# Kernel optimization log

Measured on AMD Instinct MI355X. Metric: run time of the kernel, lower is better.

The kernel has to match this reference:

```python
import jax, jax.numpy as jnp
import numpy as np

N_QUBITS = 4
N_LAYERS = 2
_I2 = jnp.eye(2, dtype=jnp.complex64)
_X = jnp.array([[0.0, 1.0], [1.0, 0.0]], dtype=jnp.complex64)


def _apply_1q_batched(state, U, wire):
    # state: [B,2,2,2,2] complex, U: [B,2,2] (per-sample gate)
    s = jnp.moveaxis(state, 1 + wire, -1)
    s = jnp.einsum('bij,b...j->b...i', U, s)
    return jnp.moveaxis(s, -1, 1 + wire)


def _apply_1q(state, U, wire):
    # shared 2x2 gate on `wire`
    s = jnp.moveaxis(state, 1 + wire, -1)
    s = jnp.einsum('ij,...j->...i', U, s)
    return jnp.moveaxis(s, -1, 1 + wire)


def _apply_cnot(state, c, t):
    s = jnp.moveaxis(state, (1 + c, 1 + t), (-2, -1))  # [...,2(ctrl),2(tgt)]
    s = jnp.stack([s[..., 0, :], s[..., 1, ::-1]], axis=-2)  # flip target if ctrl=1
    return jnp.moveaxis(s, (-2, -1), (1 + c, 1 + t))


def _rot_matrix(phi, theta, omega):
    # qml.Rot = RZ(omega) @ RY(theta) @ RZ(phi)
    c, s = jnp.cos(theta / 2), jnp.sin(theta / 2)
    ep = jnp.exp(-0.5j * (phi + omega))  # e^{-i(phi+omega)/2}
    em = jnp.exp(-0.5j * (phi - omega))  # e^{-i(phi-omega)/2}
    return jnp.stack([
        jnp.stack([ep * c, -jnp.conj(em) * s]),
        jnp.stack([em * s, jnp.conj(ep) * c]),
    ]).astype(jnp.complex64)


def _circuit(angles, weights):
    # angles: [B, 4] real; weights: [2, 4, 3] real -> [B, 4] PauliZ expvals
    B = angles.shape[0]
    state = jnp.zeros((B,) + (2,) * N_QUBITS, jnp.complex64)
    state = state.at[(slice(None),) + (0,) * N_QUBITS].set(1.0)  # |0000>
    # AngleEmbedding (rotation='X'): RX(angle_w) on wire w, batched over samples
    for w in range(N_QUBITS):
        half = angles[:, w] / 2
        c, s = jnp.cos(half), jnp.sin(half)
        U = c[:, None, None] * _I2 - 1j * s[:, None, None] * _X  # [B,2,2]
        state = _apply_1q_batched(state, U, w)
    # StronglyEntanglingLayers: Rot on each wire, then ring of CNOTs with range r
    for l in range(N_LAYERS):
        for w in range(N_QUBITS):
            U = _rot_matrix(weights[l, w, 0], weights[l, w, 1], weights[l, w, 2])
            state = _apply_1q(state, U, w)
        r = (l % (N_QUBITS - 1)) + 1  # PennyLane default ranges
        for w in range(N_QUBITS):
            state = _apply_cnot(state, w, (w + r) % N_QUBITS)
    probs = state.real ** 2 + state.imag ** 2  # [B,2,2,2,2]
    z = []
    for w in range(N_QUBITS):
        other = tuple(a for a in range(1, N_QUBITS + 1) if a != 1 + w)
        p = probs.sum(other)  # [B,2]
        z.append(p[:, 0] - p[:, 1])
    return jnp.stack(z, axis=-1)  # [B,4]


def setup_inputs() -> dict:
    key = jax.random.key(0)
    ks = jax.random.split(key, 6)
    B, D_IN, D_OUT, NQ = 65536, 512, 512, N_QUBITS
    x = jax.random.normal(ks[0], (B, D_IN), jnp.float32)
    pre_W = jax.random.normal(ks[1], (NQ, D_IN), jnp.float32) / np.sqrt(D_IN)
    pre_b = jax.random.normal(ks[2], (NQ,), jnp.float32) * 0.05
    weights = jax.random.uniform(ks[3], (N_LAYERS, NQ, 3), jnp.float32) * (2 * np.pi)
    post_W = jax.random.normal(ks[4], (D_OUT, NQ), jnp.float32) / np.sqrt(NQ)
    post_b = jax.random.normal(ks[5], (D_OUT,), jnp.float32) * 0.05
    return {"x": x, "pre_W": pre_W, "pre_b": pre_b, "weights": weights,
            "post_W": post_W, "post_b": post_b}


def reference(x, pre_W, pre_b, weights, post_W, post_b):
    angles = jnp.tanh(x @ pre_W.T + pre_b) * jnp.pi  # [B,4]
    q = _circuit(angles, weights)                    # [B,4]
    return q @ post_W.T + post_b                     # [B,512]
```

## Files before the change

### kernel.cpp

```cpp
#include <hip/hip_runtime.h>
#include <math.h>

#define PI_F 3.14159265358979323846f


typedef float floatx4 __attribute__((ext_vector_type(4)));

static __device__ __forceinline__ void st_store4(float* p, floatx4 v)
{
    *reinterpret_cast<floatx4*>(p) = v;
}

static __device__ __forceinline__ float fast_tanh(float a)
{
    a = fminf(fmaxf(a, -15.f), 15.f);
    const float e = __expf(2.f * a);
    return (e - 1.f) / (e + 1.f);
}

template<int ST>
__device__ __forceinline__ void rot_inlane(float* ar, float* ai,
    float u00r, float u00i, float u01r, float u01i,
    float u10r, float u10i, float u11r, float u11i)
{
#pragma unroll
    for (int k = 0; k < 4; ++k) {
        if (k & ST) continue;
        const int j = k | ST;
        const float Ar = ar[k], Ai = ai[k], Br = ar[j], Bi = ai[j];
        ar[k] = u00r*Ar - u00i*Ai + u01r*Br - u01i*Bi;
        ai[k] = u00r*Ai + u00i*Ar + u01r*Bi + u01i*Br;
        ar[j] = u10r*Ar - u10i*Ai + u11r*Br - u11i*Bi;
        ai[j] = u10r*Ai + u10i*Ar + u11r*Bi + u11i*Br;
    }
}

template<int XM>
__device__ __forceinline__ void rot_cross(float* ar, float* ai, bool ownB,
    float u00r, float u00i, float u01r, float u01i,
    float u10r, float u10i, float u11r, float u11i)
{
    const float cAr = ownB ? u11r : u00r;
    const float cAi = ownB ? u11i : u00i;
    const float cBr = ownB ? u10r : u01r;
    const float cBi = ownB ? u10i : u01i;
#pragma unroll
    for (int k = 0; k < 4; ++k) {
        const float pr = __shfl_xor(ar[k], XM, 64);
        const float pi = __shfl_xor(ai[k], XM, 64);
        const float vr = ar[k], vi = ai[k];
        ar[k] = cAr*vr - cAi*vi + cBr*pr - cBi*pi;
        ai[k] = cAr*vi + cAi*vr + cBr*pi + cBi*pr;
    }
}

#define ROT_COEFFS(L, W) \
    const float ph = wts[((L)*4+(W))*3+0]; \
    const float th = wts[((L)*4+(W))*3+1]; \
    const float om = wts[((L)*4+(W))*3+2]; \
    const float s_  = __sinf(0.5f*th),        c_  = __cosf(0.5f*th); \
    const float sp_ = __sinf(0.5f*(ph+om)),   cp_ = __cosf(0.5f*(ph+om)); \
    const float sq_ = __sinf(0.5f*(ph-om)),   cq_ = __cosf(0.5f*(ph-om));

#define U_ARGS cp_*c_, -sp_*c_, -cq_*s_, -sq_*s_, cq_*s_, -sq_*s_, cp_*c_, sp_*c_

__global__ __launch_bounds__(256) void k_fused(
    const float* __restrict__ x,
    const float* __restrict__ preW,
    const float* __restrict__ preb,
    const float* __restrict__ wts,
    const float* __restrict__ postW,
    const float* __restrict__ postb,
    float* __restrict__ out, int B)
{
    const int lane  = threadIdx.x & 63;
    const int wid   = threadIdx.x >> 6;
    const int base  = blockIdx.x * 64;
    const int wbase = base + wid * 16;
    if (base >= B) return;

    float4 wA[4], wB[4];
#pragma unroll
    for (int w = 0; w < 4; ++w) {
        wA[w] = *reinterpret_cast<const float4*>(preW + w * 512 + lane * 4);
        wB[w] = *reinterpret_cast<const float4*>(preW + w * 512 + 256 + lane * 4);
    }
    const float4 pb = *reinterpret_cast<const float4*>(preb);
    const float pb01 = (lane & 1) ? pb.y : pb.x;
    const float pb23 = (lane & 1) ? pb.w : pb.z;
    const float pbv  = (lane & 2) ? pb23 : pb01;

    float a[4];
#pragma unroll
    for (int p = 0; p < 4; ++p) {
        const int b0 = wbase + p * 4;

        float4 xa[4], xb[4];
#pragma unroll
        for (int t = 0; t < 4; ++t) {
            const float* xr = x + (size_t)(b0 + t) * 512;
            xa[t] = *reinterpret_cast<const float4*>(xr + lane * 4);
            xb[t] = *reinterpret_cast<const float4*>(xr + 256 + lane * 4);
        }

        float acc[4][4];
#pragma unroll
        for (int t = 0; t < 4; ++t) {
#pragma unroll
            for (int w = 0; w < 4; ++w) {
                acc[t][w] = xa[t].x * wA[w].x + xa[t].y * wA[w].y + xa[t].z * wA[w].z + xa[t].w * wA[w].w
                          + xb[t].x * wB[w].x + xb[t].y * wB[w].y + xb[t].z * wB[w].z + xb[t].w * wB[w].w;
            }
        }

        float v[4];
#pragma unroll
        for (int t = 0; t < 4; ++t) {
            float a01 = (lane & 1) ? acc[t][1] : acc[t][0];
            float b01 = (lane & 1) ? acc[t][0] : acc[t][1];
            a01 += __shfl_xor(b01, 1, 64);
            float a23 = (lane & 1) ? acc[t][3] : acc[t][2];
            float b23 = (lane & 1) ? acc[t][2] : acc[t][3];
            a23 += __shfl_xor(b23, 1, 64);
            const float vv = (lane & 2) ? a23 : a01;
            const float uu = (lane & 2) ? a01 : a23;
            v[t] = vv + __shfl_xor(uu, 2, 64);
        }
        float c01 = (lane & 4) ? v[1] : v[0];
        float d01 = (lane & 4) ? v[0] : v[1];
        c01 += __shfl_xor(d01, 4, 64);
        float c23 = (lane & 4) ? v[3] : v[2];
        float d23 = (lane & 4) ? v[2] : v[3];
        c23 += __shfl_xor(d23, 4, 64);
        float m = (lane & 8) ? c23 : c01;
        float n = (lane & 8) ? c01 : c23;
        m += __shfl_xor(n, 8, 64);
        m += __shfl_xor(m, 16, 64);
        m += __shfl_xor(m, 32, 64);

        a[p] = fast_tanh(m + pbv) * PI_F;
    }

    const float comb = (lane & 32) ? ((lane & 16) ? a[3] : a[2])
                                   : ((lane & 16) ? a[1] : a[0]);
    const int sb = (lane & 48) + 4 * ((lane >> 2) & 3);
    const float A0 = __shfl(comb, sb + 0, 64);
    const float A1 = __shfl(comb, sb + 1, 64);
    const float A2 = __shfl(comb, sb + 2, 64);
    const float A3 = __shfl(comb, sb + 3, 64);

    const bool lb3 = (lane & 2) != 0;
    const bool lb2 = (lane & 1) != 0;

    const float s0 = __sinf(0.5f * A0), c0 = __cosf(0.5f * A0);
    const float s1 = __sinf(0.5f * A1), c1 = __cosf(0.5f * A1);
    const float s2 = __sinf(0.5f * A2), c2 = __cosf(0.5f * A2);
    const float s3 = __sinf(0.5f * A3), c3 = __cosf(0.5f * A3);

    const float mhi = (lb3 ? s0 : c0) * (lb2 ? s1 : c1);
    const float hr  = lb3 ? (lb2 ? -mhi : 0.f) : (lb2 ? 0.f : mhi);
    const float hi  = (lb3 != lb2) ? -mhi : 0.f;
    const float low0 = c2 * c3, low1 = c2 * s3, low2 = s2 * c3, low3 = s2 * s3;

    float ar[4], ai[4];
    ar[0] =  hr * low0;  ai[0] =  hi * low0;
    ar[1] =  hi * low1;  ai[1] = -hr * low1;
    ar[2] =  hi * low2;  ai[2] = -hr * low2;
    ar[3] = -hr * low3;  ai[3] = -hi * low3;

    { ROT_COEFFS(0, 0); rot_cross<2>(ar, ai, lb3, U_ARGS); }
    { ROT_COEFFS(0, 1); rot_cross<1>(ar, ai, lb2, U_ARGS); }
    { ROT_COEFFS(0, 2); rot_inlane<2>(ar, ai, U_ARGS); }
    { ROT_COEFFS(0, 3); rot_inlane<1>(ar, ai, U_ARGS); }

    {
#pragma unroll
        for (int k = 0; k < 4; ++k) {
            const float tr = __shfl_xor(ar[k], 1, 64);
            const float ti = __shfl_xor(ai[k], 1, 64);
            ar[k] = lb3 ? tr : ar[k];
            ai[k] = lb3 ? ti : ai[k];
        }
    }
    {
        const float t0r = ar[0], t0i = ai[0], t1r = ar[1], t1i = ai[1];
        ar[0] = lb2 ? ar[2] : ar[0];  ai[0] = lb2 ? ai[2] : ai[0];
        ar[1] = lb2 ? ar[3] : ar[1];  ai[1] = lb2 ? ai[3] : ai[1];
        ar[2] = lb2 ? t0r   : ar[2];  ai[2] = lb2 ? t0i   : ai[2];
        ar[3] = lb2 ? t1r   : ar[3];  ai[3] = lb2 ? t1i   : ai[3];
    }
    {
        float t;
        t = ar[2]; ar[2] = ar[3]; ar[3] = t;
        t = ai[2]; ai[2] = ai[3]; ai[3] = t;
    }
    {
        ar[1] = __shfl_xor(ar[1], 2, 64);  ai[1] = __shfl_xor(ai[1], 2, 64);
        ar[3] = __shfl_xor(ar[3], 2, 64);  ai[3] = __shfl_xor(ai[3], 2, 64);
    }

    { ROT_COEFFS(1, 0); rot_cross<2>(ar, ai, lb3, U_ARGS); }
    { ROT_COEFFS(1, 1); rot_cross<1>(ar, ai, lb2, U_ARGS); }
    { ROT_COEFFS(1, 2); rot_inlane<2>(ar, ai, U_ARGS); }
    { ROT_COEFFS(1, 3); rot_inlane<1>(ar, ai, U_ARGS); }

    {
        const float t0r = ar[0], t0i = ai[0], t1r = ar[1], t1i = ai[1];
        ar[0] = lb3 ? ar[2] : ar[0];  ai[0] = lb3 ? ai[2] : ai[0];
        ar[1] = lb3 ? ar[3] : ar[1];  ai[1] = lb3 ? ai[3] : ai[1];
        ar[2] = lb3 ? t0r   : ar[2];  ai[2] = lb3 ? t0i   : ai[2];
        ar[3] = lb3 ? t1r   : ar[3];  ai[3] = lb3 ? t1i   : ai[3];
    }
    {
        const float t0r = ar[0], t0i = ai[0], t2r = ar[2], t2i = ai[2];
        ar[0] = lb2 ? ar[1] : ar[0];  ai[0] = lb2 ? ai[1] : ai[0];
        ar[1] = lb2 ? t0r   : ar[1];  ai[1] = lb2 ? t0i   : ai[1];
        ar[2] = lb2 ? ar[3] : ar[2];  ai[2] = lb2 ? ai[3] : ai[2];
        ar[3] = lb2 ? t2r   : ar[3];  ai[3] = lb2 ? t2i   : ai[3];
    }
    {
        ar[2] = __shfl_xor(ar[2], 2, 64);  ai[2] = __shfl_xor(ai[2], 2, 64);
        ar[3] = __shfl_xor(ar[3], 2, 64);  ai[3] = __shfl_xor(ai[3], 2, 64);
    }
    {
        ar[1] = __shfl_xor(ar[1], 1, 64);  ai[1] = __shfl_xor(ai[1], 1, 64);
        ar[3] = __shfl_xor(ar[3], 1, 64);  ai[3] = __shfl_xor(ai[3], 1, 64);
    }

    const float p0 = ar[0]*ar[0] + ai[0]*ai[0];
    const float p1 = ar[1]*ar[1] + ai[1]*ai[1];
    const float p2 = ar[2]*ar[2] + ai[2]*ai[2];
    const float p3 = ar[3]*ar[3] + ai[3]*ai[3];
    const float s01 = p0 + p1, s23 = p2 + p3;
    const float sum = s01 + s23;
    float z0 = lb3 ? -sum : sum;
    float z1 = lb2 ? -sum : sum;
    float z2 = s01 - s23;
    float z3 = (p0 - p1) + (p2 - p3);
    z0 += __shfl_xor(z0, 1, 64);  z0 += __shfl_xor(z0, 2, 64);
    z1 += __shfl_xor(z1, 1, 64);  z1 += __shfl_xor(z1, 2, 64);
    z2 += __shfl_xor(z2, 1, 64);  z2 += __shfl_xor(z2, 2, 64);
    z3 += __shfl_xor(z3, 1, 64);  z3 += __shfl_xor(z3, 2, 64);

    const float4* pW4 = reinterpret_cast<const float4*>(postW);
    const float4* pb4 = reinterpret_cast<const float4*>(postb);
    const float4 q0w = pW4[4 * lane + 0], q1w = pW4[4 * lane + 1];
    const float4 q2w = pW4[4 * lane + 2], q3w = pW4[4 * lane + 3];
    const float4 q4w = pW4[4 * (64 + lane) + 0], q5w = pW4[4 * (64 + lane) + 1];
    const float4 q6w = pW4[4 * (64 + lane) + 2], q7w = pW4[4 * (64 + lane) + 3];
    const float4 bb0 = pb4[lane], bb1 = pb4[64 + lane];

#pragma unroll
    for (int s = 0; s < 16; ++s) {
        const float q0 = __shfl(z0, s * 4, 64);
        const float q1 = __shfl(z1, s * 4, 64);
        const float q2 = __shfl(z2, s * 4, 64);
        const float q3 = __shfl(z3, s * 4, 64);
        floatx4 o0, o1;
        o0.x = fmaf(q3, q0w.w, fmaf(q2, q0w.z, fmaf(q1, q0w.y, fmaf(q0, q0w.x, bb0.x))));
        o0.y = fmaf(q3, q1w.w, fmaf(q2, q1w.z, fmaf(q1, q1w.y, fmaf(q0, q1w.x, bb0.y))));
        o0.z = fmaf(q3, q2w.w, fmaf(q2, q2w.z, fmaf(q1, q2w.y, fmaf(q0, q2w.x, bb0.z))));
        o0.w = fmaf(q3, q3w.w, fmaf(q2, q3w.z, fmaf(q1, q3w.y, fmaf(q0, q3w.x, bb0.w))));
        o1.x = fmaf(q3, q4w.w, fmaf(q2, q4w.z, fmaf(q1, q4w.y, fmaf(q0, q4w.x, bb1.x))));
        o1.y = fmaf(q3, q5w.w, fmaf(q2, q5w.z, fmaf(q1, q5w.y, fmaf(q0, q5w.x, bb1.y))));
        o1.z = fmaf(q3, q6w.w, fmaf(q2, q6w.z, fmaf(q1, q6w.y, fmaf(q0, q6w.x, bb1.z))));
        o1.w = fmaf(q3, q7w.w, fmaf(q2, q7w.z, fmaf(q1, q7w.y, fmaf(q0, q7w.x, bb1.w))));
        float* orow = out + (size_t)(wbase + s) * 512;
        st_store4(orow + 4 * lane, o0);
        st_store4(orow + 256 + 4 * lane, o1);
    }
}

extern "C" void kernel_launch(void* const* d_in, const int* in_sizes, int n_in,
                              void* d_out, int out_size, void* d_ws, size_t ws_size,
                              hipStream_t stream)
{
    const float* x     = (const float*)d_in[0];
    const float* preW  = (const float*)d_in[1];
    const float* preb  = (const float*)d_in[2];
    const float* wts   = (const float*)d_in[3];
    const float* postW = (const float*)d_in[4];
    const float* postb = (const float*)d_in[5];
    float* out = (float*)d_out;
    const int B = in_sizes[0] / 512;

    k_fused<<<dim3((B + 63) / 64), dim3(256), 0, stream>>>(
        x, preW, preb, wts, postW, postb, out, B);
}
```

Measured before the change: 48.10 us.

## Double-buffer x row loads and process two 16-row chunks per wave

Each wave now handles 32 rows instead of 16, split into two 16-row chunks. The x loads for the next 4-row pass are issued into a second register buffer while the current pass's dot products and reductions run, so global-load latency overlaps with compute. The per-wave weight loads are amortized over twice as many rows and the grid is halved. The cost is higher register pressure from the double buffer, which may reduce occupancy.

```diff
diff --git a/kernel.cpp b/kernel.cpp
--- a/kernel.cpp
+++ b/kernel.cpp
@@ -5,11 +5,6 @@
 
 
 typedef float floatx4 __attribute__((ext_vector_type(4)));
-
-static __device__ __forceinline__ void st_store4(float* p, floatx4 v)
-{
-    *reinterpret_cast<floatx4*>(p) = v;
-}
 
 static __device__ __forceinline__ float fast_tanh(float a)
 {
@@ -64,6 +59,55 @@
 
 #define U_ARGS cp_*c_, -sp_*c_, -cq_*s_, -sq_*s_, cq_*s_, -sq_*s_, cp_*c_, sp_*c_
 
+#define ISSUE_PASS(slot, p) { \
+    const float* xr_ = x + (size_t)(wbase + (p) * 4) * 512 + lane * 4; \
+    bxa[slot][0] = *reinterpret_cast<const float4*>(xr_); \
+    bxb[slot][0] = *reinterpret_cast<const float4*>(xr_ + 256); \
+    bxa[slot][1] = *reinterpret_cast<const float4*>(xr_ + 512); \
+    bxb[slot][1] = *reinterpret_cast<const float4*>(xr_ + 768); \
+    bxa[slot][2] = *reinterpret_cast<const float4*>(xr_ + 1024); \
+    bxb[slot][2] = *reinterpret_cast<const float4*>(xr_ + 1280); \
+    bxa[slot][3] = *reinterpret_cast<const float4*>(xr_ + 1536); \
+    bxb[slot][3] = *reinterpret_cast<const float4*>(xr_ + 1792); }
+
+#define DOTS_FOLD(slot, dest) { \
+    float acc[4][4]; \
+    _Pragma("unroll") \
+    for (int t = 0; t < 4; ++t) { \
+        _Pragma("unroll") \
+        for (int w = 0; w < 4; ++w) { \
+            acc[t][w] = bxa[slot][t].x * wA[w].x + bxa[slot][t].y * wA[w].y \
+                      + bxa[slot][t].z * wA[w].z + bxa[slot][t].w * wA[w].w \
+                      + bxb[slot][t].x * wB[w].x + bxb[slot][t].y * wB[w].y \
+                      + bxb[slot][t].z * wB[w].z + bxb[slot][t].w * wB[w].w; \
+        } \
+    } \
+    float v[4]; \
+    _Pragma("unroll") \
+    for (int t = 0; t < 4; ++t) { \
+        float a01 = (lane & 1) ? acc[t][1] : acc[t][0]; \
+        float b01 = (lane & 1) ? acc[t][0] : acc[t][1]; \
+        a01 += __shfl_xor(b01, 1, 64); \
+        float a23 = (lane & 1) ? acc[t][3] : acc[t][2]; \
+        float b23 = (lane & 1) ? acc[t][2] : acc[t][3]; \
+        a23 += __shfl_xor(b23, 1, 64); \
+        const float vv = (lane & 2) ? a23 : a01; \
+        const float uu = (lane & 2) ? a01 : a23; \
+        v[t] = vv + __shfl_xor(uu, 2, 64); \
+    } \
+    float c01 = (lane & 4) ? v[1] : v[0]; \
+    float d01 = (lane & 4) ? v[0] : v[1]; \
+    c01 += __shfl_xor(d01, 4, 64); \
+    float c23 = (lane & 4) ? v[3] : v[2]; \
+    float d23 = (lane & 4) ? v[2] : v[3]; \
+    c23 += __shfl_xor(d23, 4, 64); \
+    float m_ = (lane & 8) ? c23 : c01; \
+    float n_ = (lane & 8) ? c01 : c23; \
+    m_ += __shfl_xor(n_, 8, 64); \
+    m_ += __shfl_xor(m_, 16, 64); \
+    m_ += __shfl_xor(m_, 32, 64); \
+    dest = fast_tanh(m_ + pbv) * PI_F; }
+
 __global__ __launch_bounds__(256) void k_fused(
     const float* __restrict__ x,
     const float* __restrict__ preW,
@@ -75,9 +119,8 @@
 {
     const int lane  = threadIdx.x & 63;
     const int wid   = threadIdx.x >> 6;
-    const int base  = blockIdx.x * 64;
-    const int wbase = base + wid * 16;
-    if (base >= B) return;
+    const int wbase = blockIdx.x * 128 + wid * 32;
+    if (wbase >= B) return;
 
     float4 wA[4], wB[4];
 #pragma unroll
@@ -90,158 +133,6 @@
     const float pb23 = (lane & 1) ? pb.w : pb.z;
     const float pbv  = (lane & 2) ? pb23 : pb01;
 
-    float a[4];
-#pragma unroll
-    for (int p = 0; p < 4; ++p) {
-        const int b0 = wbase + p * 4;
-
-        float4 xa[4], xb[4];
-#pragma unroll
-        for (int t = 0; t < 4; ++t) {
-            const float* xr = x + (size_t)(b0 + t) * 512;
-            xa[t] = *reinterpret_cast<const float4*>(xr + lane * 4);
-            xb[t] = *reinterpret_cast<const float4*>(xr + 256 + lane * 4);
-        }
-
-        float acc[4][4];
-#pragma unroll
-        for (int t = 0; t < 4; ++t) {
-#pragma unroll
-            for (int w = 0; w < 4; ++w) {
-                acc[t][w] = xa[t].x * wA[w].x + xa[t].y * wA[w].y + xa[t].z * wA[w].z + xa[t].w * wA[w].w
-                          + xb[t].x * wB[w].x + xb[t].y * wB[w].y + xb[t].z * wB[w].z + xb[t].w * wB[w].w;
-            }
-        }
-
-        float v[4];
-#pragma unroll
-        for (int t = 0; t < 4; ++t) {
-            float a01 = (lane & 1) ? acc[t][1] : acc[t][0];
-            float b01 = (lane & 1) ? acc[t][0] : acc[t][1];
-            a01 += __shfl_xor(b01, 1, 64);
-            float a23 = (lane & 1) ? acc[t][3] : acc[t][2];
-            float b23 = (lane & 1) ? acc[t][2] : acc[t][3];
-            a23 += __shfl_xor(b23, 1, 64);
-            const float vv = (lane & 2) ? a23 : a01;
-            const float uu = (lane & 2) ? a01 : a23;
-            v[t] = vv + __shfl_xor(uu, 2, 64);
-        }
-        float c01 = (lane & 4) ? v[1] : v[0];
-        float d01 = (lane & 4) ? v[0] : v[1];
-        c01 += __shfl_xor(d01, 4, 64);
-        float c23 = (lane & 4) ? v[3] : v[2];
-        float d23 = (lane & 4) ? v[2] : v[3];
-        c23 += __shfl_xor(d23, 4, 64);
-        float m = (lane & 8) ? c23 : c01;
-        float n = (lane & 8) ? c01 : c23;
-        m += __shfl_xor(n, 8, 64);
-        m += __shfl_xor(m, 16, 64);
-        m += __shfl_xor(m, 32, 64);
-
-        a[p] = fast_tanh(m + pbv) * PI_F;
-    }
-
-    const float comb = (lane & 32) ? ((lane & 16) ? a[3] : a[2])
-                                   : ((lane & 16) ? a[1] : a[0]);
-    const int sb = (lane & 48) + 4 * ((lane >> 2) & 3);
-    const float A0 = __shfl(comb, sb + 0, 64);
-    const float A1 = __shfl(comb, sb + 1, 64);
-    const float A2 = __shfl(comb, sb + 2, 64);
-    const float A3 = __shfl(comb, sb + 3, 64);
-
-    const bool lb3 = (lane & 2) != 0;
-    const bool lb2 = (lane & 1) != 0;
-
-    const float s0 = __sinf(0.5f * A0), c0 = __cosf(0.5f * A0);
-    const float s1 = __sinf(0.5f * A1), c1 = __cosf(0.5f * A1);
-    const float s2 = __sinf(0.5f * A2), c2 = __cosf(0.5f * A2);
-    const float s3 = __sinf(0.5f * A3), c3 = __cosf(0.5f * A3);
-
-    const float mhi = (lb3 ? s0 : c0) * (lb2 ? s1 : c1);
-    const float hr  = lb3 ? (lb2 ? -mhi : 0.f) : (lb2 ? 0.f : mhi);
-    const float hi  = (lb3 != lb2) ? -mhi : 0.f;
-    const float low0 = c2 * c3, low1 = c2 * s3, low2 = s2 * c3, low3 = s2 * s3;
-
-    float ar[4], ai[4];
-    ar[0] =  hr * low0;  ai[0] =  hi * low0;
-    ar[1] =  hi * low1;  ai[1] = -hr * low1;
-    ar[2] =  hi * low2;  ai[2] = -hr * low2;
-    ar[3] = -hr * low3;  ai[3] = -hi * low3;
-
-    { ROT_COEFFS(0, 0); rot_cross<2>(ar, ai, lb3, U_ARGS); }
-    { ROT_COEFFS(0, 1); rot_cross<1>(ar, ai, lb2, U_ARGS); }
-    { ROT_COEFFS(0, 2); rot_inlane<2>(ar, ai, U_ARGS); }
-    { ROT_COEFFS(0, 3); rot_inlane<1>(ar, ai, U_ARGS); }
-
-    {
-#pragma unroll
-        for (int k = 0; k < 4; ++k) {
-            const float tr = __shfl_xor(ar[k], 1, 64);
-            const float ti = __shfl_xor(ai[k], 1, 64);
-            ar[k] = lb3 ? tr : ar[k];
-            ai[k] = lb3 ? ti : ai[k];
-        }
-    }
-    {
-        const float t0r = ar[0], t0i = ai[0], t1r = ar[1], t1i = ai[1];
-        ar[0] = lb2 ? ar[2] : ar[0];  ai[0] = lb2 ? ai[2] : ai[0];
-        ar[1] = lb2 ? ar[3] : ar[1];  ai[1] = lb2 ? ai[3] : ai[1];
-        ar[2] = lb2 ? t0r   : ar[2];  ai[2] = lb2 ? t0i   : ai[2];
-        ar[3] = lb2 ? t1r   : ar[3];  ai[3] = lb2 ? t1i   : ai[3];
-    }
-    {
-        float t;
-        t = ar[2]; ar[2] = ar[3]; ar[3] = t;
-        t = ai[2]; ai[2] = ai[3]; ai[3] = t;
-    }
-    {
-        ar[1] = __shfl_xor(ar[1], 2, 64);  ai[1] = __shfl_xor(ai[1], 2, 64);
-        ar[3] = __shfl_xor(ar[3], 2, 64);  ai[3] = __shfl_xor(ai[3], 2, 64);
-    }
-
-    { ROT_COEFFS(1, 0); rot_cross<2>(ar, ai, lb3, U_ARGS); }
-    { ROT_COEFFS(1, 1); rot_cross<1>(ar, ai, lb2, U_ARGS); }
-    { ROT_COEFFS(1, 2); rot_inlane<2>(ar, ai, U_ARGS); }
-    { ROT_COEFFS(1, 3); rot_inlane<1>(ar, ai, U_ARGS); }
-
-    {
-        const float t0r = ar[0], t0i = ai[0], t1r = ar[1], t1i = ai[1];
-        ar[0] = lb3 ? ar[2] : ar[0];  ai[0] = lb3 ? ai[2] : ai[0];
-        ar[1] = lb3 ? ar[3] : ar[1];  ai[1] = lb3 ? ai[3] : ai[1];
-        ar[2] = lb3 ? t0r   : ar[2];  ai[2] = lb3 ? t0i   : ai[2];
-        ar[3] = lb3 ? t1r   : ar[3];  ai[3] = lb3 ? t1i   : ai[3];
-    }
-    {
-        const float t0r = ar[0], t0i = ai[0], t2r = ar[2], t2i = ai[2];
-        ar[0] = lb2 ? ar[1] : ar[0];  ai[0] = lb2 ? ai[1] : ai[0];
-        ar[1] = lb2 ? t0r   : ar[1];  ai[1] = lb2 ? t0i   : ai[1];
-        ar[2] = lb2 ? ar[3] : ar[2];  ai[2] = lb2 ? ai[3] : ai[2];
-        ar[3] = lb2 ? t2r   : ar[3];  ai[3] = lb2 ? t2i   : ai[3];
-    }
-    {
-        ar[2] = __shfl_xor(ar[2], 2, 64);  ai[2] = __shfl_xor(ai[2], 2, 64);
-        ar[3] = __shfl_xor(ar[3], 2, 64);  ai[3] = __shfl_xor(ai[3], 2, 64);
-    }
-    {
-        ar[1] = __shfl_xor(ar[1], 1, 64);  ai[1] = __shfl_xor(ai[1], 1, 64);
-        ar[3] = __shfl_xor(ar[3], 1, 64);  ai[3] = __shfl_xor(ai[3], 1, 64);
-    }
-
-    const float p0 = ar[0]*ar[0] + ai[0]*ai[0];
-    const float p1 = ar[1]*ar[1] + ai[1]*ai[1];
-    const float p2 = ar[2]*ar[2] + ai[2]*ai[2];
-    const float p3 = ar[3]*ar[3] + ai[3]*ai[3];
-    const float s01 = p0 + p1, s23 = p2 + p3;
-    const float sum = s01 + s23;
-    float z0 = lb3 ? -sum : sum;
-    float z1 = lb2 ? -sum : sum;
-    float z2 = s01 - s23;
-    float z3 = (p0 - p1) + (p2 - p3);
-    z0 += __shfl_xor(z0, 1, 64);  z0 += __shfl_xor(z0, 2, 64);
-    z1 += __shfl_xor(z1, 1, 64);  z1 += __shfl_xor(z1, 2, 64);
-    z2 += __shfl_xor(z2, 1, 64);  z2 += __shfl_xor(z2, 2, 64);
-    z3 += __shfl_xor(z3, 1, 64);  z3 += __shfl_xor(z3, 2, 64);
-
     const float4* pW4 = reinterpret_cast<const float4*>(postW);
     const float4* pb4 = reinterpret_cast<const float4*>(postb);
     const float4 q0w = pW4[4 * lane + 0], q1w = pW4[4 * lane + 1];
@@ -250,25 +141,143 @@
     const float4 q6w = pW4[4 * (64 + lane) + 2], q7w = pW4[4 * (64 + lane) + 3];
     const float4 bb0 = pb4[lane], bb1 = pb4[64 + lane];
 
-#pragma unroll
-    for (int s = 0; s < 16; ++s) {
-        const float q0 = __shfl(z0, s * 4, 64);
-        const float q1 = __shfl(z1, s * 4, 64);
-        const float q2 = __shfl(z2, s * 4, 64);
-        const float q3 = __shfl(z3, s * 4, 64);
-        floatx4 o0, o1;
-        o0.x = fmaf(q3, q0w.w, fmaf(q2, q0w.z, fmaf(q1, q0w.y, fmaf(q0, q0w.x, bb0.x))));
-        o0.y = fmaf(q3, q1w.w, fmaf(q2, q1w.z, fmaf(q1, q1w.y, fmaf(q0, q1w.x, bb0.y))));
-        o0.z = fmaf(q3, q2w.w, fmaf(q2, q2w.z, fmaf(q1, q2w.y, fmaf(q0, q2w.x, bb0.z))));
-        o0.w = fmaf(q3, q3w.w, fmaf(q2, q3w.z, fmaf(q1, q3w.y, fmaf(q0, q3w.x, bb0.w))));
-        o1.x = fmaf(q3, q4w.w, fmaf(q2, q4w.z, fmaf(q1, q4w.y, fmaf(q0, q4w.x, bb1.x))));
-        o1.y = fmaf(q3, q5w.w, fmaf(q2, q5w.z, fmaf(q1, q5w.y, fmaf(q0, q5w.x, bb1.y))));
-        o1.z = fmaf(q3, q6w.w, fmaf(q2, q6w.z, fmaf(q1, q6w.y, fmaf(q0, q6w.x, bb1.z))));
-        o1.w = fmaf(q3, q7w.w, fmaf(q2, q7w.z, fmaf(q1, q7w.y, fmaf(q0, q7w.x, bb1.w))));
-        float* orow = out + (size_t)(wbase + s) * 512;
-        st_store4(orow + 4 * lane, o0);
-        st_store4(orow + 256 + 4 * lane, o1);
-    }
+    const bool lb3 = (lane & 2) != 0;
+    const bool lb2 = (lane & 1) != 0;
+    const int  sb  = (lane & 48) + 4 * ((lane >> 2) & 3);
+
+    float4 bxa[2][4], bxb[2][4];
+
+    auto chunk_body = [&](int cb, float a0, float a1, float a2, float a3) {
+        const float comb = (lane & 32) ? ((lane & 16) ? a3 : a2)
+                                       : ((lane & 16) ? a1 : a0);
+        const float A0 = __shfl(comb, sb + 0, 64);
+        const float A1 = __shfl(comb, sb + 1, 64);
+        const float A2 = __shfl(comb, sb + 2, 64);
+        const float A3 = __shfl(comb, sb + 3, 64);
+
+        const float s0 = __sinf(0.5f * A0), c0 = __cosf(0.5f * A0);
+        const float s1 = __sinf(0.5f * A1), c1 = __cosf(0.5f * A1);
+        const float s2 = __sinf(0.5f * A2), c2 = __cosf(0.5f * A2);
+        const float s3 = __sinf(0.5f * A3), c3 = __cosf(0.5f * A3);
+
+        const float mhi = (lb3 ? s0 : c0) * (lb2 ? s1 : c1);
+        const float hr  = lb3 ? (lb2 ? -mhi : 0.f) : (lb2 ? 0.f : mhi);
+        const float hi  = (lb3 != lb2) ? -mhi : 0.f;
+        const float low0 = c2 * c3, low1 = c2 * s3, low2 = s2 * c3, low3 = s2 * s3;
+
+        float ar[4], ai[4];
+        ar[0] =  hr * low0;  ai[0] =  hi * low0;
+        ar[1] =  hi * low1;  ai[1] = -hr * low1;
+        ar[2] =  hi * low2;  ai[2] = -hr * low2;
+        ar[3] = -hr * low3;  ai[3] = -hi * low3;
+
+        { ROT_COEFFS(0, 0); rot_cross<2>(ar, ai, lb3, U_ARGS); }
+        { ROT_COEFFS(0, 1); rot_cross<1>(ar, ai, lb2, U_ARGS); }
+        { ROT_COEFFS(0, 2); rot_inlane<2>(ar, ai, U_ARGS); }
+        { ROT_COEFFS(0, 3); rot_inlane<1>(ar, ai, U_ARGS); }
+        {
+#pragma unroll
+            for (int k = 0; k < 4; ++k) {
+                const float tr = __shfl_xor(ar[k], 1, 64);
+                const float ti = __shfl_xor(ai[k], 1, 64);
+                ar[k] = lb3 ? tr : ar[k];
+                ai[k] = lb3 ? ti : ai[k];
+            }
+        }
+        {
+            const float t0r = ar[0], t0i = ai[0], t1r = ar[1], t1i = ai[1];
+            ar[0] = lb2 ? ar[2] : ar[0];  ai[0] = lb2 ? ai[2] : ai[0];
+            ar[1] = lb2 ? ar[3] : ar[1];  ai[1] = lb2 ? ai[3] : ai[1];
+            ar[2] = lb2 ? t0r   : ar[2];  ai[2] = lb2 ? t0i   : ai[2];
+            ar[3] = lb2 ? t1r   : ar[3];  ai[3] = lb2 ? t1i   : ai[3];
+        }
+        {
+            float t;
+            t = ar[2]; ar[2] = ar[3]; ar[3] = t;
+            t = ai[2]; ai[2] = ai[3]; ai[3] = t;
+        }
+        {
+            ar[1] = __shfl_xor(ar[1], 2, 64);  ai[1] = __shfl_xor(ai[1], 2, 64);
+            ar[3] = __shfl_xor(ar[3], 2, 64);  ai[3] = __shfl_xor(ai[3], 2, 64);
+        }
+
+        { ROT_COEFFS(1, 0); rot_cross<2>(ar, ai, lb3, U_ARGS); }
+        { ROT_COEFFS(1, 1); rot_cross<1>(ar, ai, lb2, U_ARGS); }
+        { ROT_COEFFS(1, 2); rot_inlane<2>(ar, ai, U_ARGS); }
+        { ROT_COEFFS(1, 3); rot_inlane<1>(ar, ai, U_ARGS); }
+        {
+            const float t0r = ar[0], t0i = ai[0], t1r = ar[1], t1i = ai[1];
+            ar[0] = lb3 ? ar[2] : ar[0];  ai[0] = lb3 ? ai[2] : ai[0];
+            ar[1] = lb3 ? ar[3] : ar[1];  ai[1] = lb3 ? ai[3] : ai[1];
+            ar[2] = lb3 ? t0r   : ar[2];  ai[2] = lb3 ? t0i   : ai[2];
+            ar[3] = lb3 ? t1r   : ar[3];  ai[3] = lb3 ? t1i   : ai[3];
+        }
+        {
+            const float t0r = ar[0], t0i = ai[0], t2r = ar[2], t2i = ai[2];
+            ar[0] = lb2 ? ar[1] : ar[0];  ai[0] = lb2 ? ai[1] : ai[0];
+            ar[1] = lb2 ? t0r   : ar[1];  ai[1] = lb2 ? t0i   : ai[1];
+            ar[2] = lb2 ? ar[3] : ar[2];  ai[2] = lb2 ? ai[3] : ai[2];
+            ar[3] = lb2 ? t2r   : ar[3];  ai[3] = lb2 ? t2i   : ai[3];
+        }
+        {
+            ar[2] = __shfl_xor(ar[2], 2, 64);  ai[2] = __shfl_xor(ai[2], 2, 64);
+            ar[3] = __shfl_xor(ar[3], 2, 64);  ai[3] = __shfl_xor(ai[3], 2, 64);
+        }
+        {
+            ar[1] = __shfl_xor(ar[1], 1, 64);  ai[1] = __shfl_xor(ai[1], 1, 64);
+            ar[3] = __shfl_xor(ar[3], 1, 64);  ai[3] = __shfl_xor(ai[3], 1, 64);
+        }
+
+        const float p0 = ar[0]*ar[0] + ai[0]*ai[0];
+        const float p1 = ar[1]*ar[1] + ai[1]*ai[1];
+        const float p2 = ar[2]*ar[2] + ai[2]*ai[2];
+        const float p3 = ar[3]*ar[3] + ai[3]*ai[3];
+        const float s01 = p0 + p1, s23 = p2 + p3;
+        const float sum = s01 + s23;
+        float z0 = lb3 ? -sum : sum;
+        float z1 = lb2 ? -sum : sum;
+        float z2 = s01 - s23;
+        float z3 = (p0 - p1) + (p2 - p3);
+        z0 += __shfl_xor(z0, 1, 64);  z0 += __shfl_xor(z0, 2, 64);
+        z1 += __shfl_xor(z1, 1, 64);  z1 += __shfl_xor(z1, 2, 64);
+        z2 += __shfl_xor(z2, 1, 64);  z2 += __shfl_xor(z2, 2, 64);
+        z3 += __shfl_xor(z3, 1, 64);  z3 += __shfl_xor(z3, 2, 64);
+
+#pragma unroll
+        for (int s = 0; s < 16; ++s) {
+            const float q0 = __shfl(z0, s * 4, 64);
+            const float q1 = __shfl(z1, s * 4, 64);
+            const float q2 = __shfl(z2, s * 4, 64);
+            const float q3 = __shfl(z3, s * 4, 64);
+            floatx4 o0, o1;
+            o0.x = fmaf(q3, q0w.w, fmaf(q2, q0w.z, fmaf(q1, q0w.y, fmaf(q0, q0w.x, bb0.x))));
+            o0.y = fmaf(q3, q1w.w, fmaf(q2, q1w.z, fmaf(q1, q1w.y, fmaf(q0, q1w.x, bb0.y))));
+            o0.z = fmaf(q3, q2w.w, fmaf(q2, q2w.z, fmaf(q1, q2w.y, fmaf(q0, q2w.x, bb0.z))));
+            o0.w = fmaf(q3, q3w.w, fmaf(q2, q3w.z, fmaf(q1, q3w.y, fmaf(q0, q3w.x, bb0.w))));
+            o1.x = fmaf(q3, q4w.w, fmaf(q2, q4w.z, fmaf(q1, q4w.y, fmaf(q0, q4w.x, bb1.x))));
+            o1.y = fmaf(q3, q5w.w, fmaf(q2, q5w.z, fmaf(q1, q5w.y, fmaf(q0, q5w.x, bb1.y))));
+            o1.z = fmaf(q3, q6w.w, fmaf(q2, q6w.z, fmaf(q1, q6w.y, fmaf(q0, q6w.x, bb1.z))));
+            o1.w = fmaf(q3, q7w.w, fmaf(q2, q7w.z, fmaf(q1, q7w.y, fmaf(q0, q7w.x, bb1.w))));
+            float* orow = out + (size_t)(cb + s) * 512;
+            *reinterpret_cast<floatx4*>(orow + 4 * lane) = o0;
+            *reinterpret_cast<floatx4*>(orow + 256 + 4 * lane) = o1;
+        }
+    };
+
+    float a0, a1, a2, a3;
+
+    ISSUE_PASS(0, 0);
+    ISSUE_PASS(1, 1);
+    DOTS_FOLD(0, a0);  ISSUE_PASS(0, 2);
+    DOTS_FOLD(1, a1);  ISSUE_PASS(1, 3);
+    DOTS_FOLD(0, a2);  ISSUE_PASS(0, 4);
+    DOTS_FOLD(1, a3);  ISSUE_PASS(1, 5);
+    chunk_body(wbase, a0, a1, a2, a3);
+    DOTS_FOLD(0, a0);  ISSUE_PASS(0, 6);
+    DOTS_FOLD(1, a1);  ISSUE_PASS(1, 7);
+    DOTS_FOLD(0, a2);
+    DOTS_FOLD(1, a3);
+    chunk_body(wbase + 16, a0, a1, a2, a3);
 }
 
 extern "C" void kernel_launch(void* const* d_in, const int* in_sizes, int n_in,
@@ -284,6 +293,6 @@
     float* out = (float*)d_out;
     const int B = in_sizes[0] / 512;
 
-    k_fused<<<dim3((B + 63) / 64), dim3(256), 0, stream>>>(
+    k_fused<<<dim3((B + 127) / 128), dim3(256), 0, stream>>>(
         x, preW, preb, wts, postW, postb, out, B);
 }
```

Measured after the change: 48.59 us. About the same (+1.0%).
